# Optimization experiments

Hardware: AMD Instinct MI355X
Metric: run time of the kernel (lower is better)

Reference implementation:

```python
import jax, jax.numpy as jnp
import numpy as np

K = 32  # k-th nearest neighbor (excluding self), matches KDistanceDetector(k=32)


def setup_inputs() -> dict:
    key = jax.random.key(0)
    B, D = 16384, 128
    images = jax.random.normal(key, (B, D), dtype=jnp.float32)
    return {"images": images}


def reference(images):
    # model is identity: vision_features = images, shape [B, D]
    x = images
    # torch.cdist p=2 with mm path: sq dists via gram matrix
    sq_norms = jnp.sum(x * x, axis=1)                      # [B]
    sq = sq_norms[:, None] + sq_norms[None, :] - 2.0 * (x @ x.T)  # [B, B]
    sq = jnp.maximum(sq, 0.0)
    B = x.shape[0]
    # Mask out the diagonal (self-distance). Original removes it and views
    # [B, B-1]; setting it to +inf before sorting yields the identical k-th
    # smallest value (inf sorts last), and keeps sqrt grads clean.
    diag = jnp.eye(B, dtype=bool)
    sq = jnp.where(diag, jnp.inf, sq)
    d = jnp.sqrt(sq)                                       # [B, B]
    a = jnp.sort(d, axis=1)                                # full per-row sort, as in original
    return a[:, K]                                         # [B]
```

## Files before the change

kernel.cpp:

```cpp
#include <hip/hip_runtime.h>


typedef unsigned short u16;
typedef unsigned int   u32;
typedef __attribute__((ext_vector_type(8))) u16    ushort8;
typedef __attribute__((ext_vector_type(8))) __bf16 bf16x8;
typedef __attribute__((ext_vector_type(4))) float  f32x4;
typedef __attribute__((ext_vector_type(4))) u32    u32x4;

#define NB   16384
#define ND   128
#define NSEG 32
#define SCAP 12
#define NTH  33
#define ZWH  (-2.62f)
#define NEGF (-3.0e38f)
#define POSF ( 3.0e38f)

#define OFF_X    ((size_t)0)
#define OFF_NORM (OFF_X    + (size_t)NB * ND * 2)
#define OFF_TACC (OFF_NORM + (size_t)NB * 4)
#define OFF_XBAR (OFF_TACC + (size_t)NB * 4)
#define OFF_SCAL (OFF_XBAR + 512)
#define OFF_CNTS (OFF_SCAL + 256)
#define OFF_CAND (OFF_CNTS + (size_t)NB * NSEG * 4)

static __device__ __forceinline__ u16 f2bf(float f) {
  u32 u = __float_as_uint(f);
  u32 r = u + 0x7FFFu + ((u >> 16) & 1u);
  return (u16)(r >> 16);
}
static __device__ __forceinline__ float bf2f(u16 h) {
  return __uint_as_float(((u32)h) << 16);
}

#if defined(__has_builtin)
#if __has_builtin(__builtin_amdgcn_global_load_lds)
#define HAVE_GLDS 1
#endif
#endif

static __device__ __forceinline__ void stage16(const u16* gsrc_lane,
                                               u16* lds_base, int l) {
#ifdef HAVE_GLDS
  __builtin_amdgcn_global_load_lds(
      (const __attribute__((address_space(1))) void*)gsrc_lane,
      (__attribute__((address_space(3))) void*)lds_base, 16, 0, 0);
#else
  *(ushort8*)(lds_base + l * 8) = *(const ushort8*)gsrc_lane;
#endif
}
static __device__ __forceinline__ void stage4(const float* gsrc_lane,
                                              float* lds_base, int l) {
#ifdef HAVE_GLDS
  __builtin_amdgcn_global_load_lds(
      (const __attribute__((address_space(1))) void*)gsrc_lane,
      (__attribute__((address_space(3))) void*)lds_base, 4, 0, 0);
#else
  lds_base[l] = *gsrc_lane;
#endif
}

__global__ void k_prep(const float* __restrict__ x, u16* __restrict__ X,
                       float* __restrict__ norms, float* xbar, float* scal) {
  if (blockIdx.x == 0) {
    int tt = threadIdx.x;
    if (tt < 128) xbar[tt] = 0.f;
    if (tt < 2)   scal[tt] = 0.f;
  }
  int w = threadIdx.x >> 6, l = threadIdx.x & 63;
  int r = blockIdx.x * 4 + w;
  const float2* xr2 = (const float2*)(x + (size_t)r * ND);
  float2 a = xr2[l];
  u16 h0 = f2bf(a.x), h1 = f2bf(a.y);
  float b0 = bf2f(h0), b1 = bf2f(h1);
  float n = b0 * b0 + b1 * b1;
#pragma unroll
  for (int off = 1; off < 64; off <<= 1) n += __shfl_xor(n, off, 64);
  *(u32*)(X + (size_t)r * ND + 2 * l) = (u32)h0 | ((u32)h1 << 16);
  if (l == 0) norms[r] = n;
}

__global__ void k_stats(const u16* __restrict__ X, const float* __restrict__ norms,
                        float* xbar, float* scal) {
  __shared__ float xs[2][128];
  __shared__ float red1[256], red2[256];
  int t = threadIdx.x, col = t & 127, half = t >> 7;
  int rbase = blockIdx.x * 256 + half * 128;
  float acc = 0.f;
  for (int rr = 0; rr < 128; ++rr)
    acc += bf2f(X[(size_t)(rbase + rr) * ND + col]);
  xs[half][col] = acc;
  float ln = norms[blockIdx.x * 256 + t];
  red1[t] = ln; red2[t] = ln * ln;
  __syncthreads();
  for (int s = 128; s > 0; s >>= 1) {
    if (t < s) { red1[t] += red1[t + s]; red2[t] += red2[t + s]; }
    __syncthreads();
  }
  if (t == 0) { atomicAdd(&scal[0], red1[0]); atomicAdd(&scal[1], red2[0]); }
  if (t < 128) atomicAdd(&xbar[t], xs[0][t] + xs[1][t]);
}

__global__ void k_thresh(const u16* __restrict__ X, const float* __restrict__ norms,
                         const float* __restrict__ xbar, const float* __restrict__ scal,
                         float* __restrict__ tacc) {
  __shared__ float xb[128];
  int t = threadIdx.x;
  if (t < 128) xb[t] = xbar[t] * (1.0f / NB);
  __syncthreads();
  int r = blockIdx.x * 256 + t;
  float n = norms[r];
  const u16* xr = X + (size_t)r * ND;
  float dot = 0.f;
#pragma unroll
  for (int c8 = 0; c8 < 16; ++c8) {
    ushort8 v = *(const ushort8*)(xr + c8 * 8);
#pragma unroll
    for (int j = 0; j < 8; ++j) dot += bf2f(v[j]) * xb[c8 * 8 + j];
  }
  float nbar = scal[0] * (1.0f / NB);
  float Vn = fmaxf(scal[1] * (1.0f / NB) - nbar * nbar, 0.f);
  float m = n + nbar - 2.f * dot;
  float v = Vn + 4.f * n * (nbar / ND);
  float nu = 2.f * m * m / v;
  float cc = v / (2.f * m);
  float a1 = 2.f / (9.f * nu);
  float inner = 1.f - a1 + ZWH * sqrtf(a1);
  float tsq = cc * nu * inner * inner * inner;
  tacc[r] = 0.5f * (n - tsq);
}

#define FILTER_TILE(DGC)                                                      \
  _Pragma("unroll") for (int i = 0; i < 4; ++i) {                             \
    _Pragma("unroll") for (int j = 0; j < 4; ++j) {                           \
      _Pragma("unroll") for (int v = 0; v < 4; ++v) {                         \
        float val = acc[i][j][v] - nch4[i][v];                                \
        bool p = (val >= tj[j]);                                              \
        if (DGC) p = p && ((c0 + wc * 64 + i * 16 + lq * 4 + v) != rj[j]);    \
        if (p) {                                                              \
          u32 c = cnt4[j];                                                    \
          if (c < SCAP) cands[segb[j] + c] = val;                             \
          cnt4[j] = c + 1;                                                    \
        }                                                                     \
      }                                                                       \
    }                                                                         \
  }

__global__ __launch_bounds__(256, 2) void k_gram(
    const u16* __restrict__ X, const float* __restrict__ norms,
    const float* __restrict__ tacc, u32* __restrict__ counts,
    float* __restrict__ cands) {
  __shared__ u16 ldsA[2][32 * 512];
  __shared__ __align__(16) float nchs[2][128];
  const int bid = blockIdx.x;
  const int logical = (bid & 7) * 64 + (bid >> 3);
  const int q = logical >> 7, strip = logical & 127;
  const int r0 = strip * 128;
  const int t = threadIdx.x, w = t >> 6, l = t & 63;
  const int wr = w & 1, wc = w >> 1;
  const int lm = l & 15, lq = l >> 4;
  const int koff = lq * 8;

  bf16x8 bfrag[4][4];
#pragma unroll
  for (int k = 0; k < 4; ++k)
#pragma unroll
    for (int j = 0; j < 4; ++j)
      bfrag[k][j] = __builtin_bit_cast(bf16x8, *(const ushort8*)(
          X + (size_t)(r0 + (wr * 4 + j) * 16 + lm) * ND + k * 32 + koff));

  int rj[4]; float tj[4]; u32 cnt4[4]; u32 segb[4];
#pragma unroll
  for (int j = 0; j < 4; ++j) {
    rj[j] = r0 + (wr * 4 + j) * 16 + lm;
    tj[j] = tacc[rj[j]];
    cnt4[j] = 0;
    segb[j] = (u32)(rj[j] * NSEG + q * 8 + wc * 4 + lq) * SCAP;
  }

  {
    const int c0 = q * 4096;
#pragma unroll
    for (int s = 0; s < 8; ++s) {
      int g = w * 8 + s;
      stage16(X + (size_t)(c0 + (g & 7) * 16 + lm) * ND + (g >> 3) * 32 + koff,
              &ldsA[0][g * 512], l);
    }
    if (w < 2) stage4(norms + c0 + w * 64 + l, &nchs[0][w * 64], l);
  }
  __syncthreads();

  for (int it = 0; it < 32; ++it) {
    const int cur = it & 1;
    const int c0 = q * 4096 + it * 128;
    if (it + 1 < 32) {
      const int c1 = c0 + 128;
      u16* dstA = ldsA[cur ^ 1];
#pragma unroll
      for (int s = 0; s < 8; ++s) {
        int g = w * 8 + s;
        stage16(X + (size_t)(c1 + (g & 7) * 16 + lm) * ND + (g >> 3) * 32 + koff,
                &dstA[g * 512], l);
      }
      if (w < 2) stage4(norms + c1 + w * 64 + l, &nchs[cur ^ 1][w * 64], l);
    }
    __builtin_amdgcn_sched_barrier(0);

    f32x4 acc[4][4];
#pragma unroll
    for (int i = 0; i < 4; ++i)
#pragma unroll
      for (int j = 0; j < 4; ++j) acc[i][j] = (f32x4){0.f, 0.f, 0.f, 0.f};

    const u16* srcA = ldsA[cur];
#pragma unroll
    for (int k = 0; k < 4; ++k) {
      bf16x8 af[4];
#pragma unroll
      for (int i = 0; i < 4; ++i)
        af[i] = __builtin_bit_cast(bf16x8,
                 *(const ushort8*)(&srcA[(k * 8 + wc * 4 + i) * 512 + l * 8]));
#pragma unroll
      for (int i = 0; i < 4; ++i)
#pragma unroll
        for (int j = 0; j < 4; ++j)
          acc[i][j] = __builtin_amdgcn_mfma_f32_16x16x32_bf16(af[i], bfrag[k][j], acc[i][j], 0, 0, 0);
    }

    f32x4 nch4[4];
#pragma unroll
    for (int i = 0; i < 4; ++i) {
      nch4[i] = *(const f32x4*)(&nchs[cur][wc * 64 + i * 16 + lq * 4]);
      nch4[i] = nch4[i] * 0.5f;
    }

    if (c0 == r0) { FILTER_TILE(true) } else { FILTER_TILE(false) }

    __syncthreads();
  }
#pragma unroll
  for (int j = 0; j < 4; ++j)
    counts[rj[j] * NSEG + q * 8 + wc * 4 + lq] = cnt4[j];
}

__global__ void k_select(const u32* __restrict__ counts, const float* __restrict__ cands,
                         const float* __restrict__ norms, float* __restrict__ out) {
  int w = threadIdx.x >> 6, l = threadIdx.x & 63;
  int r = blockIdx.x * 4 + w;
  u32 myc = (l < NSEG) ? counts[r * NSEG + l] : 0u;
  u32 tot = myc, mx = myc;
#pragma unroll
  for (int off = 1; off < 64; off <<= 1) {
    tot += __shfl_xor(tot, off, 64);
    u32 o = (u32)__shfl_xor((int)mx, off, 64);
    mx = mx > o ? mx : o;
  }
  if (tot < NTH || mx > SCAP) return;

  const float* base = cands + (size_t)r * (NSEG * SCAP);
  float v0, v1, v2, v3, v4, v5;
#define LOADV(e, dst)                                        \
  {                                                          \
    int f = l + 64 * e;                                      \
    int sg = f / SCAP, sl = f - sg * SCAP;                   \
    u32 c = (u32)__shfl((int)myc, sg, 64);                   \
    float x = base[f];                                       \
    dst = (sl < (int)c) ? x : NEGF;                          \
  }
  LOADV(0, v0) LOADV(1, v1) LOADV(2, v2) LOADV(3, v3) LOADV(4, v4) LOADV(5, v5)
#undef LOADV

  float last = NEGF;
  for (int e = 0; e < NTH; ++e) {
    float m = fmaxf(fmaxf(fmaxf(v0, v1), fmaxf(v2, v3)), fmaxf(v4, v5));
#pragma unroll
    for (int off = 1; off < 64; off <<= 1) m = fmaxf(m, __shfl_xor(m, off, 64));
    bool mine = (v0 == m) || (v1 == m) || (v2 == m) || (v3 == m) || (v4 == m) || (v5 == m);
    unsigned long long bal = __ballot(mine);
    int owner = __ffsll(bal) - 1;
    if (l == owner) {
      if      (v0 == m) v0 = NEGF;
      else if (v1 == m) v1 = NEGF;
      else if (v2 == m) v2 = NEGF;
      else if (v3 == m) v3 = NEGF;
      else if (v4 == m) v4 = NEGF;
      else              v5 = NEGF;
    }
    last = m;
  }
  out[r] = sqrtf(fmaxf(norms[r] - 2.f * last, 0.f));
}

__global__ void k_fallback(const u32* __restrict__ counts, const u16* __restrict__ X,
                           const float* __restrict__ norms, float* __restrict__ out) {
  __shared__ float sq[NB];
  __shared__ float xr[ND];
  __shared__ float rmin[256];
  __shared__ int   ridx[256];
  __shared__ int   nbad;
  __shared__ int   badlist[256];
  int t = threadIdx.x;
  if (t == 0) nbad = 0;
  __syncthreads();
  int r = blockIdx.x * 256 + t;
  u32 tot = 0, mx = 0;
#pragma unroll
  for (int s4 = 0; s4 < 8; ++s4) {
    u32x4 c = *(const u32x4*)(counts + (size_t)r * NSEG + s4 * 4);
#pragma unroll
    for (int u = 0; u < 4; ++u) { tot += c[u]; mx = c[u] > mx ? c[u] : mx; }
  }
  if (tot < NTH || mx > SCAP) { int p = atomicAdd(&nbad, 1); badlist[p] = r; }
  __syncthreads();
  int nb = nbad;
  for (int ii = 0; ii < nb; ++ii) {
    int rr = badlist[ii];
    if (t < 128) xr[t] = bf2f(X[(size_t)rr * ND + t]);
    __syncthreads();
    float n_r = norms[rr];
    for (int jj = 0; jj < 64; ++jj) {
      int j = t + 256 * jj;
      const u16* xj = X + (size_t)j * ND;
      float dot = 0.f;
#pragma unroll
      for (int c8 = 0; c8 < 16; ++c8) {
        ushort8 vv = *(const ushort8*)(xj + c8 * 8);
#pragma unroll
        for (int u = 0; u < 8; ++u) dot += bf2f(vv[u]) * xr[c8 * 8 + u];
      }
      sq[j] = (j == rr) ? POSF : fmaxf(n_r + norms[j] - 2.f * dot, 0.f);
    }
    __syncthreads();
    float last = 0.f;
    for (int e = 0; e < NTH; ++e) {
      float lm = POSF; int li = -1;
      for (int jj = 0; jj < 64; ++jj) {
        int j = t + 256 * jj;
        float s = sq[j];
        if (s < lm) { lm = s; li = j; }
      }
      rmin[t] = lm; ridx[t] = li;
      __syncthreads();
      if (t == 0) {
        float gm = POSF; int gi = -1;
        for (int u = 0; u < 256; ++u)
          if (rmin[u] < gm) { gm = rmin[u]; gi = ridx[u]; }
        sq[gi] = POSF;
        rmin[0] = gm;
      }
      __syncthreads();
      last = rmin[0];
      __syncthreads();
    }
    if (t == 0) out[rr] = sqrtf(fmaxf(last, 0.f));
    __syncthreads();
  }
}

extern "C" void kernel_launch(void* const* d_in, const int* in_sizes, int n_in,
                              void* d_out, int out_size, void* d_ws, size_t ws_size,
                              hipStream_t stream) {
  const float* x = (const float*)d_in[0];
  float* out = (float*)d_out;
  char* ws = (char*)d_ws;
  u16*   X     = (u16*)  (ws + OFF_X);
  float* norms = (float*)(ws + OFF_NORM);
  float* tacc  = (float*)(ws + OFF_TACC);
  float* xbar  = (float*)(ws + OFF_XBAR);
  float* scal  = (float*)(ws + OFF_SCAL);
  u32*   cnts  = (u32*)  (ws + OFF_CNTS);
  float* cands = (float*)(ws + OFF_CAND);

  k_prep    <<<4096, 256, 0, stream>>>(x, X, norms, xbar, scal);
  k_stats   <<<64,   256, 0, stream>>>(X, norms, xbar, scal);
  k_thresh  <<<64,   256, 0, stream>>>(X, norms, xbar, scal, tacc);
  k_gram    <<<512,  256, 0, stream>>>(X, norms, tacc, cnts, cands);
  k_select  <<<4096, 256, 0, stream>>>(cnts, cands, norms, out);
  k_fallback<<<64,   256, 0, stream>>>(cnts, X, norms, out);
}
```

Before: 200.2 us.

## Vectorize stats reduction, add early-out filter test, and tree-reduce fallback selection

The stats kernel now loads 8 bf16 values per thread with vector loads and reduces partial column sums in shared memory, replacing strided scalar loads. The gram filter first checks the max of each 4-value fragment against the threshold and skips the per-element candidate logic when none passes. The fallback selection replaces a serial 256-way scan by thread 0 with a tree reduction, and only the owning thread rescans its column after a removal. These are separate local changes spread over three kernels, and the gram-filter early-out is the one most likely to matter in the hot path.

```diff
diff --git a/kernel.cpp b/kernel.cpp
--- a/kernel.cpp
+++ b/kernel.cpp
@@ -83,23 +83,34 @@
 
 __global__ void k_stats(const u16* __restrict__ X, const float* __restrict__ norms,
                         float* xbar, float* scal) {
-  __shared__ float xs[2][128];
+  __shared__ float xs[16][128];
   __shared__ float red1[256], red2[256];
-  int t = threadIdx.x, col = t & 127, half = t >> 7;
-  int rbase = blockIdx.x * 256 + half * 128;
-  float acc = 0.f;
-  for (int rr = 0; rr < 128; ++rr)
-    acc += bf2f(X[(size_t)(rbase + rr) * ND + col]);
-  xs[half][col] = acc;
-  float ln = norms[blockIdx.x * 256 + t];
+  int t = threadIdx.x;
+  int cg = t & 15;
+  int rs = t >> 4;
+  int rbase = blockIdx.x * 256;
+  float s[8] = {0.f, 0.f, 0.f, 0.f, 0.f, 0.f, 0.f, 0.f};
+  for (int rr = 0; rr < 16; ++rr) {
+    int row = rbase + rs + rr * 16;
+    ushort8 v = *(const ushort8*)(X + (size_t)row * ND + cg * 8);
+#pragma unroll
+    for (int u = 0; u < 8; ++u) s[u] += bf2f(v[u]);
+  }
+#pragma unroll
+  for (int u = 0; u < 8; ++u) xs[rs][cg * 8 + u] = s[u];
+  float ln = norms[rbase + t];
   red1[t] = ln; red2[t] = ln * ln;
   __syncthreads();
-  for (int s = 128; s > 0; s >>= 1) {
-    if (t < s) { red1[t] += red1[t + s]; red2[t] += red2[t + s]; }
+  if (t < 128) {
+    float a = 0.f;
+    for (int rsub = 0; rsub < 16; ++rsub) a += xs[rsub][t];
+    atomicAdd(&xbar[t], a);
+  }
+  for (int st = 128; st > 0; st >>= 1) {
+    if (t < st) { red1[t] += red1[t + st]; red2[t] += red2[t + st]; }
     __syncthreads();
   }
   if (t == 0) { atomicAdd(&scal[0], red1[0]); atomicAdd(&scal[1], red2[0]); }
-  if (t < 128) atomicAdd(&xbar[t], xs[0][t] + xs[1][t]);
 }
 
 __global__ void k_thresh(const u16* __restrict__ X, const float* __restrict__ norms,
@@ -130,22 +141,6 @@
   float tsq = cc * nu * inner * inner * inner;
   tacc[r] = 0.5f * (n - tsq);
 }
-
-#define FILTER_TILE(DGC)                                                      \
-  _Pragma("unroll") for (int i = 0; i < 4; ++i) {                             \
-    _Pragma("unroll") for (int j = 0; j < 4; ++j) {                           \
-      _Pragma("unroll") for (int v = 0; v < 4; ++v) {                         \
-        float val = acc[i][j][v] - nch4[i][v];                                \
-        bool p = (val >= tj[j]);                                              \
-        if (DGC) p = p && ((c0 + wc * 64 + i * 16 + lq * 4 + v) != rj[j]);    \
-        if (p) {                                                              \
-          u32 c = cnt4[j];                                                    \
-          if (c < SCAP) cands[segb[j] + c] = val;                             \
-          cnt4[j] = c + 1;                                                    \
-        }                                                                     \
-      }                                                                       \
-    }                                                                         \
-  }
 
 __global__ __launch_bounds__(256, 2) void k_gram(
     const u16* __restrict__ X, const float* __restrict__ norms,
@@ -235,7 +230,28 @@
       nch4[i] = nch4[i] * 0.5f;
     }
 
-    if (c0 == r0) { FILTER_TILE(true) } else { FILTER_TILE(false) }
+    const bool dg = (c0 == r0);
+#pragma unroll
+    for (int i = 0; i < 4; ++i) {
+#pragma unroll
+      for (int j = 0; j < 4; ++j) {
+        f32x4 val = acc[i][j] - nch4[i];
+        float g01 = fmaxf(val[0], val[1]);
+        float g23 = fmaxf(val[2], val[3]);
+        if (fmaxf(g01, g23) >= tj[j]) {
+#pragma unroll
+          for (int v = 0; v < 4; ++v) {
+            bool p = (val[v] >= tj[j]);
+            if (dg) p = p && ((c0 + wc * 64 + i * 16 + lq * 4 + v) != rj[j]);
+            if (p) {
+              u32 c = cnt4[j];
+              if (c < SCAP) cands[segb[j] + c] = val[v];
+              cnt4[j] = c + 1;
+            }
+          }
+        }
+      }
+    }
 
     __syncthreads();
   }
@@ -298,6 +314,8 @@
   __shared__ float xr[ND];
   __shared__ float rmin[256];
   __shared__ int   ridx[256];
+  __shared__ float tmin[256];
+  __shared__ int   tidx[256];
   __shared__ int   nbad;
   __shared__ int   badlist[256];
   int t = threadIdx.x;
@@ -332,25 +350,37 @@
       sq[j] = (j == rr) ? POSF : fmaxf(n_r + norms[j] - 2.f * dot, 0.f);
     }
     __syncthreads();
-    float last = 0.f;
-    for (int e = 0; e < NTH; ++e) {
-      float lm = POSF; int li = -1;
+    {
+      float lmv = POSF; int lix = -1;
       for (int jj = 0; jj < 64; ++jj) {
         int j = t + 256 * jj;
         float s = sq[j];
-        if (s < lm) { lm = s; li = j; }
-      }
-      rmin[t] = lm; ridx[t] = li;
+        if (s < lmv) { lmv = s; lix = j; }
+      }
+      rmin[t] = lmv; ridx[t] = lix;
+    }
+    __syncthreads();
+    float last = 0.f;
+    for (int e = 0; e < NTH; ++e) {
+      tmin[t] = rmin[t]; tidx[t] = ridx[t];
       __syncthreads();
-      if (t == 0) {
-        float gm = POSF; int gi = -1;
-        for (int u = 0; u < 256; ++u)
-          if (rmin[u] < gm) { gm = rmin[u]; gi = ridx[u]; }
+      for (int s = 128; s > 0; s >>= 1) {
+        if (t < s && tmin[t + s] < tmin[t]) { tmin[t] = tmin[t + s]; tidx[t] = tidx[t + s]; }
+        __syncthreads();
+      }
+      float gm = tmin[0]; int gi = tidx[0];
+      last = gm;
+      __syncthreads();
+      if (t == (gi & 255)) {
         sq[gi] = POSF;
-        rmin[0] = gm;
-      }
-      __syncthreads();
-      last = rmin[0];
+        float lmv = POSF; int lix = -1;
+        for (int jj = 0; jj < 64; ++jj) {
+          int j = t + 256 * jj;
+          float s = sq[j];
+          if (s < lmv) { lmv = s; lix = j; }
+        }
+        rmin[t] = lmv; ridx[t] = lix;
+      }
       __syncthreads();
     }
     if (t == 0) out[rr] = sqrtf(fmaxf(last, 0.f));
```

After: 215.2 us. +7.5%, slower.
